# Kernel tuning notes

Hardware: AMD Instinct MI355X
Metric: run time of the kernel (lower is better)

Reference implementation:

```python
import jax, jax.numpy as jnp
import numpy as np

N, H, T, L, D_IN, D_QK, D_V = 8, 8, 1024, 1024, 128, 128, 128


def setup_inputs() -> dict:
    key = jax.random.key(0)
    ks = jax.random.split(key, 12)
    s = 1.0 / np.sqrt(D_IN)
    sq = 1.0 / np.sqrt(D_QK)
    return {
        "X": jax.random.normal(ks[0], (N, H, L, D_IN), jnp.float32),
        "t1": jax.random.normal(ks[1], (N, T), jnp.float32),
        "Q": jax.random.normal(ks[2], (N, H, T, D_QK), jnp.float32),
        "Wk1": jax.random.normal(ks[3], (D_IN, D_QK), jnp.float32) * s,
        "bk1": jnp.zeros((D_QK,), jnp.float32),
        "Wk2": jax.random.normal(ks[4], (D_QK, D_QK), jnp.float32) * sq,
        "bk2": jnp.zeros((D_QK,), jnp.float32),
        "Wv1": jax.random.normal(ks[5], (D_IN, D_QK), jnp.float32) * s,
        "bv1": jnp.zeros((D_QK,), jnp.float32),
        "Wv2": jax.random.normal(ks[6], (D_QK, D_V), jnp.float32) * sq,
        "bv2": jnp.zeros((D_V,), jnp.float32),
        "log_tau": jnp.asarray(0.0, jnp.float32),  # log(init_tau=1)
    }


def _mlp(x, W1, b1, W2, b2):
    # MLP(d_in, [d_qk], d_out): Linear -> relu -> Linear
    return jax.nn.relu(x @ W1 + b1) @ W2 + b2


def reference(X, t1, Q, Wk1, bk1, Wk2, bk2, Wv1, bv1, Wv2, bv2, log_tau):
    t2 = X[:, 0, :, -1]                      # (N, L)
    K = _mlp(X, Wk1, bk1, Wk2, bk2)          # (N, H, L, d_qk)
    V = _mlp(X, Wv1, bv1, Wv2, bv2)          # (N, H, L, d_v)
    tau = jnp.exp(log_tau)
    # gaussian weight: -(Q.K)^2 / tau
    A = jnp.einsum('nhtc,nhlc->nhtl', Q, K)
    A = -(A * A) / tau
    mask = (t1[:, :, None] >= t2[:, None, :])[:, None, :, :]  # (N,1,T,L)
    A = jax.nn.softmax(A * mask, axis=-1) * mask
    return jnp.einsum('nhtl,nhlc->nhtc', A, V)
```

## Files before the change

### kernel.cpp

```cpp
#include <hip/hip_runtime.h>
#include <hip/hip_bf16.h>

typedef __bf16 bf16_t;
typedef _Float16 f16_t;
typedef bf16_t bf16x8 __attribute__((ext_vector_type(8)));
typedef f16_t  f16x8  __attribute__((ext_vector_type(8)));
typedef f16_t  f16x4  __attribute__((ext_vector_type(4)));
typedef float  floatx4 __attribute__((ext_vector_type(4)));
typedef float  floatx16 __attribute__((ext_vector_type(16)));
typedef bf16x8 bf16x8u __attribute__((aligned(8)));
typedef f16x8  f16x8u  __attribute__((aligned(8)));

#define DEV static __device__ __forceinline__

DEV floatx4 mfma16_bf16(bf16x8 a, bf16x8 b, floatx4 c) {
  return __builtin_amdgcn_mfma_f32_16x16x32_bf16(a, b, c, 0, 0, 0);
}
DEV floatx4 mfma16_f16(f16x8 a, f16x8 b, floatx4 c) {
  return __builtin_amdgcn_mfma_f32_16x16x32_f16(a, b, c, 0, 0, 0);
}
DEV floatx16 mfma32_bf16(bf16x8 a, bf16x8 b, floatx16 c) {
  return __builtin_amdgcn_mfma_f32_32x32x16_bf16(a, b, c, 0, 0, 0);
}
DEV floatx16 mfma32x8_f16(f16x4 a, f16x4 b, floatx16 c) {
  return __builtin_amdgcn_mfma_f32_32x32x8f16(a, b, c, 0, 0, 0);
}
DEV void async_ld16(void* lds, const void* g) {
  __builtin_amdgcn_global_load_lds(
      (const __attribute__((address_space(1))) unsigned int*)g,
      (__attribute__((address_space(3))) unsigned int*)lds, 16, 0, 0);
}
DEV float fast_exp2(float x) {
  float r;
  asm("v_exp_f32 %0, %1" : "=v"(r) : "v"(x));
  return r;
}

__global__ void prep_kernel(const float* __restrict__ Wk1, const float* __restrict__ Wk2,
                            const float* __restrict__ Wv1, const float* __restrict__ Wv2,
                            const float* __restrict__ X,
                            bf16_t* __restrict__ W1p, bf16_t* __restrict__ W2p,
                            f16_t* __restrict__ W3f, f16_t* __restrict__ W4f,
                            float* __restrict__ t2pre) {
  int b = blockIdx.x;
  if (b < 16) {
    int m = b >> 2, p = b & 3;
    const float* src = m == 0 ? Wk1 : m == 1 ? Wk2 : m == 2 ? Wv1 : Wv2;
    __shared__ float tile[32][129];
    for (int u = 0; u < 4; ++u) {
      int idx = threadIdx.x + u * 256;
      int k = idx >> 5, n4 = (idx & 31) << 2;
      float4 v = *(const float4*)(src + (size_t)(p * 32 + k) * 128 + n4);
      tile[k][n4 + 0] = v.x; tile[k][n4 + 1] = v.y;
      tile[k][n4 + 2] = v.z; tile[k][n4 + 3] = v.w;
    }
    __syncthreads();
    if (m < 2) {
      bf16_t* dst = m ? W2p : W1p;
      for (int u = 0; u < 2; ++u) {
        int idx = threadIdx.x + u * 256;
        int n = idx >> 2, kc = idx & 3;
        bf16x8 hi, lo;
        for (int j = 0; j < 8; ++j) {
          float v = tile[kc * 8 + j][n];
          bf16_t hh = (bf16_t)v;
          hi[j] = hh;
          lo[j] = (bf16_t)(v - (float)hh);
        }
        *(bf16x8*)(dst + n * 128 + p * 32 + kc * 8) = hi;
        *(bf16x8*)(dst + 16384 + n * 128 + p * 32 + kc * 8) = lo;
      }
    } else {
      f16_t* dst = (m == 3) ? W4f : W3f;
      for (int u = 0; u < 2; ++u) {
        int idx = threadIdx.x + u * 256;
        int n = idx >> 2, kc = idx & 3;
        f16x8 w;
        for (int j = 0; j < 8; ++j) w[j] = (f16_t)tile[kc * 8 + j][n];
        *(f16x8*)(dst + n * 128 + p * 32 + kc * 8) = w;
      }
    }
  } else {
    int i = (b - 16) * 256 + threadIdx.x;
    t2pre[i] = X[((size_t)(i >> 10) * 8192 + (i & 1023)) * 128 + 127];
  }
}

__global__ __launch_bounds__(256) void mlp_k_kernel(
    const float* __restrict__ X, const float* __restrict__ b1,
    const float* __restrict__ b2, const bf16_t* __restrict__ W1p,
    const bf16_t* __restrict__ W2p, bf16_t* __restrict__ Khi,
    bf16_t* __restrict__ Klo) {
  __shared__ __align__(16) char sXbuf[2 * 16896];
  __shared__ __align__(16) bf16_t sW[2][256 * 40];
  bf16_t* sXh = (bf16_t*)sXbuf;
  bf16_t* sXl = sXh + 64 * 132;

  const int tid = threadIdx.x, lane = tid & 63, wave = tid >> 6;
  const int q = lane >> 4, c15 = lane & 15;
  const size_t rowBase = (size_t)blockIdx.x * 64;

  int goff[5];
  for (int a = 0; a < 5; ++a) {
    int o = (wave + 4 * a) * 1024 + lane * 16;
    int row = o / 80, rem = o % 80;
    goff[a] = row * 256 + (rem < 64 ? rem : 0);
  }
  auto issueW = [&](int buf, int ph) {
    const bf16_t* Wp = (ph < 4) ? W1p : W2p;
    const char* base = (const char*)Wp + (ph & 3) * 64;
    for (int a = 0; a < 5; ++a)
      async_ld16((char*)sW[buf] + (wave + 4 * a) * 1024 + lane * 16, base + goff[a]);
  };

  issueW(0, 0);

  float b1v[8], b2v[8];
  for (int nt = 0; nt < 8; ++nt) { b1v[nt] = b1[nt * 16 + c15]; b2v[nt] = b2[nt * 16 + c15]; }

  for (int u = 0; u < 8; ++u) {
    int idx = tid + u * 256;
    int r = idx >> 5, c4 = (idx & 31) << 2;
    float4 v = *(const float4*)(X + (rowBase + r) * 128 + c4);
    int o = r * 132 + c4;
    float vv[4] = {v.x, v.y, v.z, v.w};
    for (int i = 0; i < 4; ++i) {
      bf16_t h = (bf16_t)vv[i];
      sXh[o + i] = h;
      sXl[o + i] = (bf16_t)(vv[i] - (float)h);
    }
  }

  floatx4 acc1[8], acc2[8];
  for (int i = 0; i < 8; ++i) { acc1[i] = {}; acc2[i] = {}; }

  __syncthreads();
#pragma unroll
  for (int ph = 0; ph < 8; ++ph) {
    if (ph < 7) issueW((ph + 1) & 1, ph + 1);
    const bf16_t* wb = sW[ph & 1];
    const int kq = ph & 3;
    floatx4* acc = (ph < 4) ? acc1 : acc2;
    const int ao = (wave * 16 + c15) * 132 + kq * 32 + q * 8;
    bf16x8 ah = *(const bf16x8u*)(sXh + ao);
    bf16x8 al = *(const bf16x8u*)(sXl + ao);
    for (int nt = 0; nt < 8; ++nt) {
      const int bo = (nt * 16 + c15) * 40 + q * 8;
      bf16x8 bh = *(const bf16x8*)(wb + bo);
      bf16x8 bl = *(const bf16x8*)(wb + 128 * 40 + bo);
      acc[nt] = mfma16_bf16(ah, bh, acc[nt]);
      acc[nt] = mfma16_bf16(ah, bl, acc[nt]);
      acc[nt] = mfma16_bf16(al, bh, acc[nt]);
    }
    if (ph == 3) {
      for (int nt = 0; nt < 8; ++nt)
        for (int r = 0; r < 4; ++r) {
          float h = fmaxf(acc1[nt][r] + b1v[nt], 0.f);
          bf16_t hh = (bf16_t)h;
          int o = (wave * 16 + q * 4 + r) * 132 + nt * 16 + c15;
          sXh[o] = hh;
          sXl[o] = (bf16_t)(h - (float)hh);
        }
    }
    __syncthreads();
  }

  for (int nt = 0; nt < 8; ++nt)
    for (int r = 0; r < 4; ++r) {
      float kv = acc2[nt][r] + b2v[nt];
      bf16_t kh = (bf16_t)kv;
      int o = (wave * 16 + q * 4 + r) * 132 + nt * 16 + c15;
      sXh[o] = kh;
      sXl[o] = (bf16_t)(kv - (float)kh);
    }
  __syncthreads();
  for (int u = 0; u < 4; ++u) {
    int idx = tid + u * 256;
    int r = idx >> 4, c8 = (idx & 15) << 3;
    bf16x8 vh = *(const bf16x8u*)(sXh + r * 132 + c8);
    bf16x8 vl = *(const bf16x8u*)(sXl + r * 132 + c8);
    *(bf16x8*)(Khi + (rowBase + r) * 128 + c8) = vh;
    *(bf16x8*)(Klo + (rowBase + r) * 128 + c8) = vl;
  }
}

__global__ __launch_bounds__(256) void mlp_v_kernel(
    const float* __restrict__ X, const float* __restrict__ b1,
    const float* __restrict__ b2, const f16_t* __restrict__ W1f,
    const f16_t* __restrict__ W2f, f16_t* __restrict__ Vt) {
  __shared__ __align__(16) f16_t sXf[64 * 136];
  __shared__ __align__(16) f16_t sW[2][128 * 40];

  const int tid = threadIdx.x, lane = tid & 63, wave = tid >> 6;
  const int q = lane >> 4, c15 = lane & 15;
  const size_t rowBase = (size_t)blockIdx.x * 64;

  int goff[3];
  for (int a = 0; a < 3; ++a) {
    int o = (wave + 4 * a) * 1024 + lane * 16;
    int row = o / 80, rem = o % 80;
    goff[a] = row * 256 + (rem < 64 ? rem : 0);
  }
  auto issueV = [&](int buf, int ph) {
    const f16_t* Wp = (ph < 4) ? W1f : W2f;
    const char* base = (const char*)Wp + (ph & 3) * 64;
    for (int a = 0; a < 3; ++a) {
      int j = wave + 4 * a;
      if (j < 10) async_ld16((char*)sW[buf] + j * 1024 + lane * 16, base + goff[a]);
    }
  };

  issueV(0, 0);

  float b1v[8], bvv[2][4];
  for (int nt = 0; nt < 8; ++nt) b1v[nt] = b1[nt * 16 + c15];
  for (int mt = 0; mt < 2; ++mt)
    for (int r = 0; r < 4; ++r)
      bvv[mt][r] = b2[(wave * 2 + mt) * 16 + q * 4 + r];

  for (int u = 0; u < 8; ++u) {
    int idx = tid + u * 256;
    int r = idx >> 5, c4 = (idx & 31) << 2;
    float4 v = *(const float4*)(X + (rowBase + r) * 128 + c4);
    int o = r * 136 + c4;
    sXf[o + 0] = (f16_t)v.x; sXf[o + 1] = (f16_t)v.y;
    sXf[o + 2] = (f16_t)v.z; sXf[o + 3] = (f16_t)v.w;
  }

  floatx4 acc1[8], acc2[2][4];
  for (int i = 0; i < 8; ++i) acc1[i] = {};
  for (int i = 0; i < 2; ++i) for (int j = 0; j < 4; ++j) acc2[i][j] = {};

  __syncthreads();
#pragma unroll
  for (int ph = 0; ph < 8; ++ph) {
    if (ph < 7) issueV((ph + 1) & 1, ph + 1);
    const f16_t* wb = sW[ph & 1];
    const int kq = ph & 3;
    if (ph < 4) {
      f16x8 a = *(const f16x8u*)(sXf + (wave * 16 + c15) * 136 + kq * 32 + q * 8);
      for (int nt = 0; nt < 8; ++nt) {
        f16x8 bb = *(const f16x8*)(wb + (nt * 16 + c15) * 40 + q * 8);
        acc1[nt] = mfma16_f16(a, bb, acc1[nt]);
      }
      if (ph == 3) {
        for (int nt = 0; nt < 8; ++nt)
          for (int r = 0; r < 4; ++r)
            sXf[(wave * 16 + q * 4 + r) * 136 + nt * 16 + c15] =
                (f16_t)fmaxf(acc1[nt][r] + b1v[nt], 0.f);
      }
    } else {
      f16x8 aw0 = *(const f16x8*)(wb + ((wave * 2 + 0) * 16 + c15) * 40 + q * 8);
      f16x8 aw1 = *(const f16x8*)(wb + ((wave * 2 + 1) * 16 + c15) * 40 + q * 8);
      for (int nt = 0; nt < 4; ++nt) {
        f16x8 bh = *(const f16x8u*)(sXf + (nt * 16 + c15) * 136 + kq * 32 + q * 8);
        acc2[0][nt] = mfma16_f16(aw0, bh, acc2[0][nt]);
        acc2[1][nt] = mfma16_f16(aw1, bh, acc2[1][nt]);
      }
    }
    __syncthreads();
  }

  f16_t* sVT = sXf;
  for (int mt = 0; mt < 2; ++mt)
    for (int nt = 0; nt < 4; ++nt)
      for (int r = 0; r < 4; ++r) {
        int c = (wave * 2 + mt) * 16 + q * 4 + r;
        sVT[c * 68 + nt * 16 + c15] = (f16_t)(acc2[mt][nt][r] + bvv[mt][r]);
      }
  __syncthreads();
  const int nh = (int)(rowBase >> 10);
  const int lB = (int)(rowBase & 1023);
  for (int u = 0; u < 4; ++u) {
    int idx = tid + u * 256;
    int c = idx >> 3, l8 = (idx & 7) << 3;
    *(f16x8*)(Vt + ((size_t)nh * 128 + c) * 1024 + lB + l8) =
        *(const f16x8u*)(sVT + c * 68 + l8);
  }
}

__global__ __launch_bounds__(512, 2) void attn_kernel(
    const float* __restrict__ Q, const float* __restrict__ t1,
    const float* __restrict__ t2pre, const float* __restrict__ ltau,
    const bf16_t* __restrict__ Khi, const bf16_t* __restrict__ Klo,
    const f16_t* __restrict__ Vt, float* __restrict__ out) {
  __shared__ __align__(16) char sBuf[3][27648];
  __shared__ __align__(16) float sT2[1024];

  const int tid = threadIdx.x, lane = tid & 63, wave = tid >> 6;
  const int h = lane >> 5, l31 = lane & 31;
  const int nh = blockIdx.x & 63;
  const int tB = (blockIdx.x >> 6) << 8;
  const int n = nh >> 3;
  const int qrow = tB + wave * 32 + l31;
  const float negc2 = -__expf(-ltau[0]) * 1.44269504f;

  const char* gp[4]; int ls[4]; int st[4];
  for (int a = 0; a < 4; ++a) {
    int j = wave + 8 * a;
    if (j >= 27) j -= 5;
    if (j < 17) {
      int o = j * 1024 + lane * 16;
      int half = o >= 8704 ? 1 : 0;
      int r2 = o - half * 8704;
      int row = r2 / 272, rem = r2 % 272;
      if (rem >= 256) rem = 0;
      gp[a] = (const char*)(half ? Klo : Khi) + ((size_t)((nh << 10) + row)) * 256 + rem;
      st[a] = 8192; ls[a] = o;
    } else {
      int o = (j - 17) * 1024 + lane * 16;
      int c = o / 80, rem = o % 80;
      if (rem >= 64) rem = 0;
      gp[a] = (const char*)Vt + ((size_t)((nh << 7) + c)) * 2048 + rem;
      st[a] = 64; ls[a] = 17408 + o;
    }
  }
  auto stage = [&](int buf) {
    for (int a = 0; a < 4; ++a) { async_ld16(sBuf[buf] + ls[a], gp[a]); gp[a] += st[a]; }
  };

  float2 t2v2 = *(const float2*)(t2pre + (n << 10) + tid * 2);
  const float t1v = t1[(n << 10) + qrow];
  bf16x8 qh[8], ql[8];
  {
    const float* qr = Q + ((size_t)(nh << 10) + qrow) * 128;
    for (int ks = 0; ks < 8; ++ks) {
      const float* p = qr + ks * 16 + h * 8;
      float4 v0 = *(const float4*)p;
      float4 v1 = *(const float4*)(p + 4);
      float vv[8] = {v0.x, v0.y, v0.z, v0.w, v1.x, v1.y, v1.z, v1.w};
      bf16x8 hi, lo;
      for (int j = 0; j < 8; ++j) {
        bf16_t hj = (bf16_t)vv[j];
        hi[j] = hj;
        lo[j] = (bf16_t)(vv[j] - (float)hj);
      }
      qh[ks] = hi;
      ql[ks] = lo;
    }
  }
  stage(0);
  stage(1);
  *(float2*)(sT2 + tid * 2) = t2v2;

  floatx16 O[4];
  for (int i = 0; i < 4; ++i) O[i] = {};
  float ds = 0.f;

  asm volatile("s_waitcnt vmcnt(4) lgkmcnt(0)" ::: "memory");
  __builtin_amdgcn_s_barrier();
  asm volatile("" ::: "memory");

  for (int it = 0; it < 32; ++it) {
    if (it < 30) stage((it + 2) % 3);
    const char* kb = sBuf[it % 3];
    const char* vb = kb + 17408;

    floatx16 S = {};
    for (int ks = 0; ks < 8; ++ks) {
      const int bo = l31 * 272 + ks * 32 + h * 16;
      bf16x8 kh_ = *(const bf16x8*)(kb + bo);
      bf16x8 kl_ = *(const bf16x8*)(kb + 8704 + bo);
      S = mfma32_bf16(kh_, qh[ks], S);
      S = mfma32_bf16(kl_, qh[ks], S);
      S = mfma32_bf16(kh_, ql[ks], S);
    }

    const float* t2b = sT2 + it * 32 + h * 4;
    for (int t = 0; t < 4; ++t) {
      float4 tv4 = *(const float4*)(t2b + t * 8);
      float tv[4] = {tv4.x, tv4.y, tv4.z, tv4.w};
      f16x4 pb;
      for (int j = 0; j < 4; ++j) {
        float s = S[4 * t + j];
        float e = fast_exp2(s * s * negc2);
        bool m = (t1v >= tv[j]);
        ds += m ? e : 1.f;
        pb[j] = (f16_t)(m ? e : 0.f);
      }
      for (int ct = 0; ct < 4; ++ct) {
        f16x4 va = *(const f16x4*)(vb + (ct * 32 + l31) * 80 + t * 16 + h * 8);
        O[ct] = mfma32x8_f16(va, pb, O[ct]);
      }
    }

    if (it < 30) {
      asm volatile("s_waitcnt vmcnt(4)" ::: "memory");
    } else if (it == 30) {
      asm volatile("s_waitcnt vmcnt(0)" ::: "memory");
    }
    if (it < 31) {
      asm volatile("" ::: "memory");
      __builtin_amdgcn_s_barrier();
      asm volatile("" ::: "memory");
    }
  }

  ds += __shfl_xor(ds, 32);
  const float inv = 1.f / ds;
  float* orow = out + ((size_t)(nh << 10) + qrow) * 128;
  for (int ct = 0; ct < 4; ++ct)
    for (int t = 0; t < 4; ++t) {
      int c = ct * 32 + 8 * t + 4 * h;
      float4 v = {O[ct][4 * t + 0] * inv, O[ct][4 * t + 1] * inv,
                  O[ct][4 * t + 2] * inv, O[ct][4 * t + 3] * inv};
      *(float4*)(orow + c) = v;
    }
}

extern "C" void kernel_launch(void* const* d_in, const int* in_sizes, int n_in,
                              void* d_out, int out_size, void* d_ws, size_t ws_size,
                              hipStream_t stream) {
  const float* X   = (const float*)d_in[0];
  const float* t1  = (const float*)d_in[1];
  const float* Q   = (const float*)d_in[2];
  const float* Wk1 = (const float*)d_in[3];
  const float* bk1 = (const float*)d_in[4];
  const float* Wk2 = (const float*)d_in[5];
  const float* bk2 = (const float*)d_in[6];
  const float* Wv1 = (const float*)d_in[7];
  const float* bv1 = (const float*)d_in[8];
  const float* Wv2 = (const float*)d_in[9];
  const float* bv2 = (const float*)d_in[10];
  const float* log_tau = (const float*)d_in[11];
  float* out = (float*)d_out;

  const size_t E = (size_t)64 * 1024 * 128;
  bf16_t* Khi = (bf16_t*)d_ws;
  bf16_t* Klo = Khi + E;
  f16_t*  Vt  = (f16_t*)(Klo + E);
  bf16_t* W1p = (bf16_t*)((char*)d_ws + 3 * E * 2);
  bf16_t* W2p = W1p + 32768;
  f16_t*  W3f = (f16_t*)(W2p + 32768);
  f16_t*  W4f = W3f + 16384;
  float*  t2pre = (float*)(W4f + 16384);

  prep_kernel<<<48, 256, 0, stream>>>(Wk1, Wk2, Wv1, Wv2, X, W1p, W2p, W3f, W4f, t2pre);
  mlp_k_kernel<<<1024, 256, 0, stream>>>(X, bk1, bk2, W1p, W2p, Khi, Klo);
  mlp_v_kernel<<<1024, 256, 0, stream>>>(X, bv1, bv2, W3f, W4f, Vt);
  attn_kernel<<<256, 512, 0, stream>>>(Q, t1, t2pre, log_tau, Khi, Klo, Vt, out);
}
```

Before: 232.4 us.

## Software-pipeline QK and PV across tiles with 4-stage buffer and XOR-swizzled K

Switches the shared-memory ring from three to four stages and changes the K tile layout from padded rows to an XOR-swizzled 256-byte row layout. The main loop is restructured so that the QK MFMAs for the next tile are interleaved with the exp/mask and PV MFMAs for the current tile, with a prologue and epilogue peeled off. The goal is to overlap the softmax ALU work with matrix-core work and reduce LDS bank conflicts without padding. In exchange the extra stage raises LDS use per block, which may affect occupancy, and the live S/Sn accumulators raise register pressure.

```diff
diff --git a/kernel.cpp b/kernel.cpp
--- a/kernel.cpp
+++ b/kernel.cpp
@@ -284,7 +284,7 @@
     const float* __restrict__ t2pre, const float* __restrict__ ltau,
     const bf16_t* __restrict__ Khi, const bf16_t* __restrict__ Klo,
     const f16_t* __restrict__ Vt, float* __restrict__ out) {
-  __shared__ __align__(16) char sBuf[3][27648];
+  __shared__ __align__(16) char sBuf[4][26624];
   __shared__ __align__(16) float sT2[1024];
 
   const int tid = threadIdx.x, lane = tid & 63, wave = tid >> 6;
@@ -298,21 +298,23 @@
   const char* gp[4]; int ls[4]; int st[4];
   for (int a = 0; a < 4; ++a) {
     int j = wave + 8 * a;
-    if (j >= 27) j -= 5;
-    if (j < 17) {
+    if (j >= 26) j -= 6;
+    if (j < 16) {
       int o = j * 1024 + lane * 16;
-      int half = o >= 8704 ? 1 : 0;
-      int r2 = o - half * 8704;
-      int row = r2 / 272, rem = r2 % 272;
-      if (rem >= 256) rem = 0;
-      gp[a] = (const char*)(half ? Klo : Khi) + ((size_t)((nh << 10) + row)) * 256 + rem;
+      int half = o >> 13;
+      int r2 = o & 8191;
+      int row = r2 >> 8;
+      int s = (r2 >> 4) & 15;
+      int g = s ^ (row & 15);
+      gp[a] = (const char*)(half ? Klo : Khi) +
+              ((size_t)((nh << 10) + row)) * 256 + (g << 4);
       st[a] = 8192; ls[a] = o;
     } else {
-      int o = (j - 17) * 1024 + lane * 16;
+      int o = (j - 16) * 1024 + lane * 16;
       int c = o / 80, rem = o % 80;
       if (rem >= 64) rem = 0;
       gp[a] = (const char*)Vt + ((size_t)((nh << 7) + c)) * 2048 + rem;
-      st[a] = 64; ls[a] = 17408 + o;
+      st[a] = 64; ls[a] = 16384 + o;
     }
   }
   auto stage = [&](int buf) {
@@ -341,6 +343,7 @@
   }
   stage(0);
   stage(1);
+  stage(2);
   *(float2*)(sT2 + tid * 2) = t2v2;
 
   floatx16 O[4];
@@ -351,22 +354,70 @@
   __builtin_amdgcn_s_barrier();
   asm volatile("" ::: "memory");
 
-  for (int it = 0; it < 32; ++it) {
-    if (it < 30) stage((it + 2) % 3);
-    const char* kb = sBuf[it % 3];
-    const char* vb = kb + 17408;
-
-    floatx16 S = {};
+  floatx16 S = {};
+  {
+    const char* kb = sBuf[0];
+#pragma unroll
     for (int ks = 0; ks < 8; ++ks) {
-      const int bo = l31 * 272 + ks * 32 + h * 16;
+      const int bo = l31 * 256 + ((((ks << 1) + h) ^ (l31 & 15)) << 4);
       bf16x8 kh_ = *(const bf16x8*)(kb + bo);
-      bf16x8 kl_ = *(const bf16x8*)(kb + 8704 + bo);
+      bf16x8 kl_ = *(const bf16x8*)(kb + 8192 + bo);
       S = mfma32_bf16(kh_, qh[ks], S);
       S = mfma32_bf16(kl_, qh[ks], S);
       S = mfma32_bf16(kh_, ql[ks], S);
     }
-
+  }
+
+  for (int it = 0; it < 31; ++it) {
+    if (it <= 28) stage((it + 3) & 3);
+    const char* vb = sBuf[it & 3] + 16384;
+    const char* kbn = sBuf[(it + 1) & 3];
     const float* t2b = sT2 + it * 32 + h * 4;
+    floatx16 Sn = {};
+#pragma unroll
+    for (int ks = 0; ks < 8; ++ks) {
+      {
+        const int bo = l31 * 256 + ((((ks << 1) + h) ^ (l31 & 15)) << 4);
+        bf16x8 kh_ = *(const bf16x8*)(kbn + bo);
+        bf16x8 kl_ = *(const bf16x8*)(kbn + 8192 + bo);
+        Sn = mfma32_bf16(kh_, qh[ks], Sn);
+        Sn = mfma32_bf16(kl_, qh[ks], Sn);
+        Sn = mfma32_bf16(kh_, ql[ks], Sn);
+      }
+      if (ks & 1) {
+        const int t = ks >> 1;
+        float4 tv4 = *(const float4*)(t2b + t * 8);
+        float tv[4] = {tv4.x, tv4.y, tv4.z, tv4.w};
+        f16x4 pb;
+        for (int j = 0; j < 4; ++j) {
+          float s = S[4 * t + j];
+          float e = fast_exp2(s * s * negc2);
+          bool m = (t1v >= tv[j]);
+          ds += m ? e : 1.f;
+          pb[j] = (f16_t)(m ? e : 0.f);
+        }
+        for (int ct = 0; ct < 4; ++ct) {
+          f16x4 va = *(const f16x4*)(vb + (ct * 32 + l31) * 80 + t * 16 + h * 8);
+          O[ct] = mfma32x8_f16(va, pb, O[ct]);
+        }
+      }
+    }
+    S = Sn;
+
+    if (it <= 28) {
+      asm volatile("s_waitcnt vmcnt(4)" ::: "memory");
+    } else if (it == 29) {
+      asm volatile("s_waitcnt vmcnt(0)" ::: "memory");
+    }
+    asm volatile("" ::: "memory");
+    __builtin_amdgcn_s_barrier();
+    asm volatile("" ::: "memory");
+  }
+
+  {
+    const char* vb = sBuf[3] + 16384;
+    const float* t2b = sT2 + 31 * 32 + h * 4;
+#pragma unroll
     for (int t = 0; t < 4; ++t) {
       float4 tv4 = *(const float4*)(t2b + t * 8);
       float tv[4] = {tv4.x, tv4.y, tv4.z, tv4.w};
@@ -382,17 +433,6 @@
         f16x4 va = *(const f16x4*)(vb + (ct * 32 + l31) * 80 + t * 16 + h * 8);
         O[ct] = mfma32x8_f16(va, pb, O[ct]);
       }
-    }
-
-    if (it < 30) {
-      asm volatile("s_waitcnt vmcnt(4)" ::: "memory");
-    } else if (it == 30) {
-      asm volatile("s_waitcnt vmcnt(0)" ::: "memory");
-    }
-    if (it < 31) {
-      asm volatile("" ::: "memory");
-      __builtin_amdgcn_s_barrier();
-      asm volatile("" ::: "memory");
     }
   }
 
```

Result: no change. 232.9 us (+0.2%).

## Halve attention block size, XOR-swizzle K/V shared tiles, raise MFMA priority

Applied to the files above, without the earlier changes.

The attention kernel now runs 512 blocks of 256 threads, each covering 128 query rows instead of 256, which gives more blocks to spread across CUs. The padded shared-memory layouts (272/80-byte row strides) are replaced by unpadded rows with XOR swizzles on both the global-load addresses and the LDS reads, to avoid bank conflicts while shrinking each stage buffer. The QK MFMA loop is wrapped in s_setprio and fully unrolled. In exchange, each K/V tile is reused across half as many query rows, so global and L2 traffic for K/V doubles.

```diff
diff --git a/kernel.cpp b/kernel.cpp
--- a/kernel.cpp
+++ b/kernel.cpp
@@ -279,47 +279,50 @@
   }
 }
 
-__global__ __launch_bounds__(512, 2) void attn_kernel(
+__global__ __launch_bounds__(256, 2) void attn_kernel(
     const float* __restrict__ Q, const float* __restrict__ t1,
     const float* __restrict__ t2pre, const float* __restrict__ ltau,
     const bf16_t* __restrict__ Khi, const bf16_t* __restrict__ Klo,
     const f16_t* __restrict__ Vt, float* __restrict__ out) {
-  __shared__ __align__(16) char sBuf[3][27648];
+  __shared__ __align__(16) char sBuf[3][24576];
   __shared__ __align__(16) float sT2[1024];
 
   const int tid = threadIdx.x, lane = tid & 63, wave = tid >> 6;
   const int h = lane >> 5, l31 = lane & 31;
   const int nh = blockIdx.x & 63;
-  const int tB = (blockIdx.x >> 6) << 8;
+  const int seg = blockIdx.x >> 6;
   const int n = nh >> 3;
-  const int qrow = tB + wave * 32 + l31;
+  const int qrow = seg * 128 + wave * 32 + l31;
   const float negc2 = -__expf(-ltau[0]) * 1.44269504f;
-
-  const char* gp[4]; int ls[4]; int st[4];
-  for (int a = 0; a < 4; ++a) {
-    int j = wave + 8 * a;
-    if (j >= 27) j -= 5;
-    if (j < 17) {
+  const int vswz = (l31 >> 1) & 3;
+
+  const char* gp[6]; int ls[6]; int st[6];
+  for (int a = 0; a < 6; ++a) {
+    int j = wave + 4 * a;
+    if (j < 16) {
       int o = j * 1024 + lane * 16;
-      int half = o >= 8704 ? 1 : 0;
-      int r2 = o - half * 8704;
-      int row = r2 / 272, rem = r2 % 272;
-      if (rem >= 256) rem = 0;
-      gp[a] = (const char*)(half ? Klo : Khi) + ((size_t)((nh << 10) + row)) * 256 + rem;
+      int half = o >> 13;
+      int r2 = o & 8191;
+      int row = r2 >> 8;
+      int s = (r2 >> 4) & 15;
+      int g = s ^ (row & 15);
+      gp[a] = (const char*)(half ? Klo : Khi) +
+              ((size_t)((nh << 10) + row)) * 256 + (g << 4);
       st[a] = 8192; ls[a] = o;
     } else {
-      int o = (j - 17) * 1024 + lane * 16;
-      int c = o / 80, rem = o % 80;
-      if (rem >= 64) rem = 0;
-      gp[a] = (const char*)Vt + ((size_t)((nh << 7) + c)) * 2048 + rem;
-      st[a] = 64; ls[a] = 17408 + o;
+      int o = (j - 16) * 1024 + lane * 16;
+      int c = o >> 6;
+      int u = (o >> 4) & 3;
+      int up = u ^ ((c >> 1) & 3);
+      gp[a] = (const char*)Vt + ((size_t)((nh << 7) + c)) * 2048 + up * 16;
+      st[a] = 64; ls[a] = 16384 + o;
     }
   }
   auto stage = [&](int buf) {
-    for (int a = 0; a < 4; ++a) { async_ld16(sBuf[buf] + ls[a], gp[a]); gp[a] += st[a]; }
+    for (int a = 0; a < 6; ++a) { async_ld16(sBuf[buf] + ls[a], gp[a]); gp[a] += st[a]; }
   };
 
-  float2 t2v2 = *(const float2*)(t2pre + (n << 10) + tid * 2);
+  float4 t2v4 = *(const float4*)(t2pre + (n << 10) + tid * 4);
   const float t1v = t1[(n << 10) + qrow];
   bf16x8 qh[8], ql[8];
   {
@@ -341,30 +344,33 @@
   }
   stage(0);
   stage(1);
-  *(float2*)(sT2 + tid * 2) = t2v2;
+  *(float4*)(sT2 + tid * 4) = t2v4;
 
   floatx16 O[4];
   for (int i = 0; i < 4; ++i) O[i] = {};
   float ds = 0.f;
 
-  asm volatile("s_waitcnt vmcnt(4) lgkmcnt(0)" ::: "memory");
+  asm volatile("s_waitcnt vmcnt(6) lgkmcnt(0)" ::: "memory");
   __builtin_amdgcn_s_barrier();
   asm volatile("" ::: "memory");
 
   for (int it = 0; it < 32; ++it) {
-    if (it < 30) stage((it + 2) % 3);
+    if (it <= 29) stage((it + 2) % 3);
     const char* kb = sBuf[it % 3];
-    const char* vb = kb + 17408;
+    const char* vb = kb + 16384;
 
     floatx16 S = {};
+    __builtin_amdgcn_s_setprio(1);
+#pragma unroll
     for (int ks = 0; ks < 8; ++ks) {
-      const int bo = l31 * 272 + ks * 32 + h * 16;
+      const int bo = l31 * 256 + ((((ks << 1) + h) ^ (l31 & 15)) << 4);
       bf16x8 kh_ = *(const bf16x8*)(kb + bo);
-      bf16x8 kl_ = *(const bf16x8*)(kb + 8704 + bo);
+      bf16x8 kl_ = *(const bf16x8*)(kb + 8192 + bo);
       S = mfma32_bf16(kh_, qh[ks], S);
       S = mfma32_bf16(kl_, qh[ks], S);
       S = mfma32_bf16(kh_, ql[ks], S);
     }
+    __builtin_amdgcn_s_setprio(0);
 
     const float* t2b = sT2 + it * 32 + h * 4;
     for (int t = 0; t < 4; ++t) {
@@ -379,13 +385,14 @@
         pb[j] = (f16_t)(m ? e : 0.f);
       }
       for (int ct = 0; ct < 4; ++ct) {
-        f16x4 va = *(const f16x4*)(vb + (ct * 32 + l31) * 80 + t * 16 + h * 8);
+        f16x4 va = *(const f16x4*)(vb + (ct * 32 + l31) * 64 +
+                                   ((t ^ vswz) << 4) + h * 8);
         O[ct] = mfma32x8_f16(va, pb, O[ct]);
       }
     }
 
-    if (it < 30) {
-      asm volatile("s_waitcnt vmcnt(4)" ::: "memory");
+    if (it <= 29) {
+      asm volatile("s_waitcnt vmcnt(6)" ::: "memory");
     } else if (it == 30) {
       asm volatile("s_waitcnt vmcnt(0)" ::: "memory");
     }
@@ -438,5 +445,5 @@
   prep_kernel<<<48, 256, 0, stream>>>(Wk1, Wk2, Wv1, Wv2, X, W1p, W2p, W3f, W4f, t2pre);
   mlp_k_kernel<<<1024, 256, 0, stream>>>(X, bk1, bk2, W1p, W2p, Khi, Klo);
   mlp_v_kernel<<<1024, 256, 0, stream>>>(X, bv1, bv2, W3f, W4f, Vt);
-  attn_kernel<<<256, 512, 0, stream>>>(Q, t1, t2pre, log_tau, Khi, Klo, Vt, out);
-}
+  attn_kernel<<<512, 256, 0, stream>>>(Q, t1, t2pre, log_tau, Khi, Klo, Vt, out);
+}
```

New measurement: 230.3 us. No clear change (-0.9%).
